# Optimization experiments

Hardware: AMD Instinct MI355X
Metric: run time of the kernel (lower is better)

## Reference

```python
import jax, jax.numpy as jnp
import numpy as np

B, S, D, H = 2, 2048, 768, 12
HD = D // H  # 64
SCALE = jnp.sqrt(jnp.float32(D / H))  # sqrt(head_dim) = 8


def setup_inputs() -> dict:
    key = jax.random.key(0)
    ks = jax.random.split(key, 11)
    s = 1.0 / np.sqrt(D)
    inp = {
        'Q': jax.random.normal(ks[0], (B, S, D), jnp.float32),
        'K': jax.random.normal(ks[1], (B, S, D), jnp.float32),
        'V': jax.random.normal(ks[2], (B, S, D), jnp.float32),
        # True = masked out (causal upper triangle), broadcast over heads
        'mask': jnp.broadcast_to(jnp.triu(jnp.ones((S, S), bool), k=1)[None, None], (B, 1, S, S)),
        'Wq': jax.random.uniform(ks[3], (D, D), jnp.float32, -s, s),
        'bq': jax.random.uniform(ks[4], (D,), jnp.float32, -s, s),
        'Wk': jax.random.uniform(ks[5], (D, D), jnp.float32, -s, s),
        'bk': jax.random.uniform(ks[6], (D,), jnp.float32, -s, s),
        'Wv': jax.random.uniform(ks[7], (D, D), jnp.float32, -s, s),
        'bv': jax.random.uniform(ks[8], (D,), jnp.float32, -s, s),
        'Wo': jax.random.uniform(ks[9], (D, D), jnp.float32, -s, s),
        'bo': jax.random.uniform(ks[10], (D,), jnp.float32, -s, s),
    }
    return inp


def _split_heads(x):  # [B,S,D] -> [B,H,S,HD]
    return x.reshape(B, S, H, HD).transpose(0, 2, 1, 3)


def reference(Q, K, V, mask, Wq, bq, Wk, bk, Wv, bv, Wo, bo):
    q = _split_heads(Q @ Wq.T + bq)
    k = _split_heads(K @ Wk.T + bk)
    v = _split_heads(V @ Wv.T + bv)
    # [B,H,S,S] attention scores
    scores = jnp.einsum('bhqd,bhkd->bhqk', q, k) / SCALE
    scores = jnp.where(mask, jnp.float32(-1e9), scores)
    weights = jax.nn.softmax(scores, axis=-1)
    attn = jnp.einsum('bhqk,bhkd->bhqd', weights, v)
    x = attn.transpose(0, 2, 1, 3).reshape(B, S, D)
    x = x @ Wo.T + bo
    return x, weights
```

## Files before the change

### kernel.cpp

```cpp
#include <hip/hip_runtime.h>

#define S_LEN 2048
#define DMODEL 768
#define NHEAD 12
#define BATCH 2
#define BHEADS (BATCH * NHEAD)
#define MROWS (BATCH * S_LEN)
#define X_ELEMS ((size_t)BATCH * S_LEN * DMODEL)
#define W_ELEMS ((size_t)BATCH * NHEAD * S_LEN * S_LEN)
#define WMAT_ELEMS ((size_t)DMODEL * DMODEL)

typedef __attribute__((ext_vector_type(8))) short bf16x8;
typedef __attribute__((ext_vector_type(4))) float f32x4;

__device__ __forceinline__ unsigned short f2bf(float f) {
    union { float f; unsigned int u; } v; v.f = f;
    unsigned int u = v.u;
    return (unsigned short)((u + 0x7FFFu + ((u >> 16) & 1u)) >> 16);
}

__device__ __forceinline__ bf16x8 pack8(float4 a, float4 b) {
    bf16x8 r;
    r[0] = (short)f2bf(a.x); r[1] = (short)f2bf(a.y);
    r[2] = (short)f2bf(a.z); r[3] = (short)f2bf(a.w);
    r[4] = (short)f2bf(b.x); r[5] = (short)f2bf(b.y);
    r[6] = (short)f2bf(b.z); r[7] = (short)f2bf(b.w);
    return r;
}

struct ConvArgs {
    const float* src[7];
    unsigned short* dst[7];
    int n[7];
};

__global__ __launch_bounds__(256) void convert_kernel(ConvArgs a) {
    int t = blockIdx.y;
    int idx = (blockIdx.x * 256 + threadIdx.x) * 8;
    if (idx >= a.n[t]) return;
    const float4* s = (const float4*)(a.src[t] + idx);
    float4 lo = s[0], hi = s[1];
    *(bf16x8*)(a.dst[t] + idx) = pack8(lo, hi);
}

__global__ __launch_bounds__(64) void proj_kernel(
    const unsigned short* __restrict__ A, const unsigned short* __restrict__ W,
    const float* __restrict__ bias, unsigned short* __restrict__ out,
    int mode, float oscale)
{
    int l = threadIdx.x;
    int bm = blockIdx.x & 127;
    int bn = blockIdx.x >> 7;
    int m0 = bm * 32, n0 = bn * 32;
    int lr = l & 15, ks = l >> 4, g = l >> 4;
    const unsigned short* ap = A + (size_t)(m0 + lr) * DMODEL + ks * 8;
    const unsigned short* bp = W + (size_t)(n0 + lr) * DMODEL + ks * 8;
    f32x4 acc00 = {0,0,0,0}, acc01 = {0,0,0,0}, acc10 = {0,0,0,0}, acc11 = {0,0,0,0};
    for (int k0 = 0; k0 < DMODEL; k0 += 32) {
        bf16x8 a0 = *(const bf16x8*)(ap + k0);
        bf16x8 a1 = *(const bf16x8*)(ap + 16 * DMODEL + k0);
        bf16x8 b0 = *(const bf16x8*)(bp + k0);
        bf16x8 b1 = *(const bf16x8*)(bp + 16 * DMODEL + k0);
        acc00 = __builtin_amdgcn_mfma_f32_16x16x32_bf16(a0, b0, acc00, 0, 0, 0);
        acc01 = __builtin_amdgcn_mfma_f32_16x16x32_bf16(a0, b1, acc01, 0, 0, 0);
        acc10 = __builtin_amdgcn_mfma_f32_16x16x32_bf16(a1, b0, acc10, 0, 0, 0);
        acc11 = __builtin_amdgcn_mfma_f32_16x16x32_bf16(a1, b1, acc11, 0, 0, 0);
    }
    f32x4 accs[2][2] = {{acc00, acc01}, {acc10, acc11}};
#pragma unroll
    for (int mi = 0; mi < 2; ++mi) {
#pragma unroll
        for (int ni = 0; ni < 2; ++ni) {
            int ng = n0 + ni * 16 + lr;
            int h = ng >> 6, d = ng & 63;
            float bv = bias[ng];
#pragma unroll
            for (int i = 0; i < 4; ++i) {
                int mg = m0 + mi * 16 + g * 4 + i;
                int b = mg >> 11, s = mg & 2047;
                float val = (accs[mi][ni][i] + bv) * oscale;
                size_t idx;
                if (mode == 0) idx = ((size_t)(b * NHEAD + h) * S_LEN + s) * 64 + d;
                else           idx = ((size_t)(b * NHEAD + h) * 64 + d) * S_LEN + s;
                out[idx] = f2bf(val);
            }
        }
    }
}

__global__ __launch_bounds__(256) void zero_upper_kernel(float* __restrict__ wts) {
    int qblk = blockIdx.x >> 5, tcol = blockIdx.x & 31;
    if (tcol <= qblk) return;
    int bh = blockIdx.y;
    int tid = threadIdx.x;
    float4 z = {0.f, 0.f, 0.f, 0.f};
    float* base = wts + ((size_t)bh * S_LEN + qblk * 64) * S_LEN + tcol * 64;
#pragma unroll
    for (int it = 0; it < 4; ++it) {
        int r = it * 16 + (tid >> 4);
        *(float4*)&base[(size_t)r * S_LEN + (tid & 15) * 4] = z;
    }
}

__global__ __launch_bounds__(256) void attn_fused_kernel(
    const unsigned short* __restrict__ qbuf, const unsigned short* __restrict__ kbuf,
    const unsigned short* __restrict__ vTbuf, float* __restrict__ wts,
    unsigned short* __restrict__ abuf)
{
    __shared__ unsigned short kt[64 * 72];
    __shared__ unsigned short vt[64 * 72];
    __shared__ unsigned short pt[4 * 16 * 72];
    int tid = threadIdx.x;
    int wid = tid >> 6, l = tid & 63;
    int qblk = blockIdx.x;
    int bh = blockIdx.y;
    int qr0 = qblk * 64 + wid * 16;
    int lr = l & 15, ks = l >> 4, g = l >> 4;

    const unsigned short* qp = qbuf + ((size_t)bh * S_LEN + qr0 + lr) * 64 + ks * 8;
    bf16x8 qf0 = *(const bf16x8*)qp;
    bf16x8 qf1 = *(const bf16x8*)(qp + 32);

    const unsigned short* ksrc = kbuf + (size_t)bh * S_LEN * 64;
    const unsigned short* vsrc = vTbuf + (size_t)bh * 64 * S_LEN;

    auto stageK = [&](int t) {
#pragma unroll
        for (int it = 0; it < 2; ++it) {
            int idx = it * 256 + tid;
            int row = idx >> 3, grp = idx & 7;
            *(bf16x8*)&kt[row * 72 + grp * 8] =
                *(const bf16x8*)&ksrc[(size_t)(t * 64 + row) * 64 + grp * 8];
        }
    };
    auto stageV = [&](int t) {
#pragma unroll
        for (int it = 0; it < 2; ++it) {
            int idx = it * 256 + tid;
            int row = idx >> 3, grp = idx & 7;
            *(bf16x8*)&vt[row * 72 + grp * 8] =
                *(const bf16x8*)&vsrc[(size_t)row * S_LEN + t * 64 + grp * 8];
        }
    };

    float m[4] = {-1e30f, -1e30f, -1e30f, -1e30f};
    float lsum[4] = {0.f, 0.f, 0.f, 0.f};

    for (int t = 0; t < qblk; ++t) {
        __syncthreads(); stageK(t); __syncthreads();
#pragma unroll
        for (int c = 0; c < 4; ++c) {
            const unsigned short* kp = &kt[(c * 16 + lr) * 72 + ks * 8];
            bf16x8 kf0 = *(const bf16x8*)kp;
            bf16x8 kf1 = *(const bf16x8*)(kp + 32);
            f32x4 acc = {0.f, 0.f, 0.f, 0.f};
            acc = __builtin_amdgcn_mfma_f32_16x16x32_bf16(qf0, kf0, acc, 0, 0, 0);
            acc = __builtin_amdgcn_mfma_f32_16x16x32_bf16(qf1, kf1, acc, 0, 0, 0);
#pragma unroll
            for (int i = 0; i < 4; ++i) m[i] = fmaxf(m[i], acc[i]);
        }
    }
    {
        __syncthreads(); stageK(qblk); __syncthreads();
#pragma unroll
        for (int c = 0; c < 4; ++c) {
            const unsigned short* kp = &kt[(c * 16 + lr) * 72 + ks * 8];
            bf16x8 kf0 = *(const bf16x8*)kp;
            bf16x8 kf1 = *(const bf16x8*)(kp + 32);
            f32x4 acc = {0.f, 0.f, 0.f, 0.f};
            acc = __builtin_amdgcn_mfma_f32_16x16x32_bf16(qf0, kf0, acc, 0, 0, 0);
            acc = __builtin_amdgcn_mfma_f32_16x16x32_bf16(qf1, kf1, acc, 0, 0, 0);
            int kcol = qblk * 64 + c * 16 + lr;
#pragma unroll
            for (int i = 0; i < 4; ++i)
                if (kcol <= qr0 + g * 4 + i) m[i] = fmaxf(m[i], acc[i]);
        }
    }
#pragma unroll
    for (int i = 0; i < 4; ++i) {
        m[i] = fmaxf(m[i], __shfl_xor(m[i], 1));
        m[i] = fmaxf(m[i], __shfl_xor(m[i], 2));
        m[i] = fmaxf(m[i], __shfl_xor(m[i], 4));
        m[i] = fmaxf(m[i], __shfl_xor(m[i], 8));
    }

    for (int t = 0; t < qblk; ++t) {
        __syncthreads(); stageK(t); __syncthreads();
#pragma unroll
        for (int c = 0; c < 4; ++c) {
            const unsigned short* kp = &kt[(c * 16 + lr) * 72 + ks * 8];
            bf16x8 kf0 = *(const bf16x8*)kp;
            bf16x8 kf1 = *(const bf16x8*)(kp + 32);
            f32x4 acc = {0.f, 0.f, 0.f, 0.f};
            acc = __builtin_amdgcn_mfma_f32_16x16x32_bf16(qf0, kf0, acc, 0, 0, 0);
            acc = __builtin_amdgcn_mfma_f32_16x16x32_bf16(qf1, kf1, acc, 0, 0, 0);
#pragma unroll
            for (int i = 0; i < 4; ++i) lsum[i] += __expf(acc[i] - m[i]);
        }
    }
    {
        __syncthreads(); stageK(qblk); __syncthreads();
#pragma unroll
        for (int c = 0; c < 4; ++c) {
            const unsigned short* kp = &kt[(c * 16 + lr) * 72 + ks * 8];
            bf16x8 kf0 = *(const bf16x8*)kp;
            bf16x8 kf1 = *(const bf16x8*)(kp + 32);
            f32x4 acc = {0.f, 0.f, 0.f, 0.f};
            acc = __builtin_amdgcn_mfma_f32_16x16x32_bf16(qf0, kf0, acc, 0, 0, 0);
            acc = __builtin_amdgcn_mfma_f32_16x16x32_bf16(qf1, kf1, acc, 0, 0, 0);
            int kcol = qblk * 64 + c * 16 + lr;
#pragma unroll
            for (int i = 0; i < 4; ++i)
                if (kcol <= qr0 + g * 4 + i) lsum[i] += __expf(acc[i] - m[i]);
        }
    }
#pragma unroll
    for (int i = 0; i < 4; ++i) {
        lsum[i] += __shfl_xor(lsum[i], 1);
        lsum[i] += __shfl_xor(lsum[i], 2);
        lsum[i] += __shfl_xor(lsum[i], 4);
        lsum[i] += __shfl_xor(lsum[i], 8);
    }
    float invl[4];
#pragma unroll
    for (int i = 0; i < 4; ++i) invl[i] = 1.0f / lsum[i];

    f32x4 oacc[4] = {{0,0,0,0},{0,0,0,0},{0,0,0,0},{0,0,0,0}};
    unsigned short* ptw = &pt[wid * 16 * 72];
    for (int t = 0; t <= qblk; ++t) {
        __syncthreads(); stageK(t); stageV(t); __syncthreads();
        bool dg = (t == qblk);
#pragma unroll
        for (int c = 0; c < 4; ++c) {
            const unsigned short* kp = &kt[(c * 16 + lr) * 72 + ks * 8];
            bf16x8 kf0 = *(const bf16x8*)kp;
            bf16x8 kf1 = *(const bf16x8*)(kp + 32);
            f32x4 acc = {0.f, 0.f, 0.f, 0.f};
            acc = __builtin_amdgcn_mfma_f32_16x16x32_bf16(qf0, kf0, acc, 0, 0, 0);
            acc = __builtin_amdgcn_mfma_f32_16x16x32_bf16(qf1, kf1, acc, 0, 0, 0);
            int kcol = t * 64 + c * 16 + lr;
#pragma unroll
            for (int i = 0; i < 4; ++i) {
                int qrow = qr0 + g * 4 + i;
                float w = (!dg || kcol <= qrow) ? __expf(acc[i] - m[i]) * invl[i] : 0.f;
                wts[((size_t)bh * S_LEN + qrow) * S_LEN + kcol] = w;
                ptw[(g * 4 + i) * 72 + c * 16 + lr] = f2bf(w);
            }
        }
        bf16x8 pa0 = *(bf16x8*)&ptw[lr * 72 + ks * 8];
        bf16x8 pa1 = *(bf16x8*)&ptw[lr * 72 + 32 + ks * 8];
#pragma unroll
        for (int dt = 0; dt < 4; ++dt) {
            bf16x8 vb0 = *(bf16x8*)&vt[(dt * 16 + lr) * 72 + ks * 8];
            bf16x8 vb1 = *(bf16x8*)&vt[(dt * 16 + lr) * 72 + 32 + ks * 8];
            oacc[dt] = __builtin_amdgcn_mfma_f32_16x16x32_bf16(pa0, vb0, oacc[dt], 0, 0, 0);
            oacc[dt] = __builtin_amdgcn_mfma_f32_16x16x32_bf16(pa1, vb1, oacc[dt], 0, 0, 0);
        }
    }
    int b = bh / NHEAD, h = bh % NHEAD;
#pragma unroll
    for (int dt = 0; dt < 4; ++dt) {
#pragma unroll
        for (int i = 0; i < 4; ++i) {
            int s = qr0 + g * 4 + i;
            abuf[(((size_t)b * S_LEN + s) * NHEAD + h) * 64 + dt * 16 + lr] = f2bf(oacc[dt][i]);
        }
    }
}

__global__ __launch_bounds__(64) void out_proj_kernel(
    const unsigned short* __restrict__ A, const unsigned short* __restrict__ W,
    const float* __restrict__ bias, float* __restrict__ out)
{
    int l = threadIdx.x;
    int bm = blockIdx.x & 127, bn = blockIdx.x >> 7;
    int m0 = bm * 32, n0 = bn * 32;
    int lr = l & 15, ks = l >> 4, g = l >> 4;
    const unsigned short* ap = A + (size_t)(m0 + lr) * DMODEL + ks * 8;
    const unsigned short* bp = W + (size_t)(n0 + lr) * DMODEL + ks * 8;
    f32x4 acc00 = {0,0,0,0}, acc01 = {0,0,0,0}, acc10 = {0,0,0,0}, acc11 = {0,0,0,0};
    for (int k0 = 0; k0 < DMODEL; k0 += 32) {
        bf16x8 a0 = *(const bf16x8*)(ap + k0);
        bf16x8 a1 = *(const bf16x8*)(ap + 16 * DMODEL + k0);
        bf16x8 b0 = *(const bf16x8*)(bp + k0);
        bf16x8 b1 = *(const bf16x8*)(bp + 16 * DMODEL + k0);
        acc00 = __builtin_amdgcn_mfma_f32_16x16x32_bf16(a0, b0, acc00, 0, 0, 0);
        acc01 = __builtin_amdgcn_mfma_f32_16x16x32_bf16(a0, b1, acc01, 0, 0, 0);
        acc10 = __builtin_amdgcn_mfma_f32_16x16x32_bf16(a1, b0, acc10, 0, 0, 0);
        acc11 = __builtin_amdgcn_mfma_f32_16x16x32_bf16(a1, b1, acc11, 0, 0, 0);
    }
    f32x4 accs[2][2] = {{acc00, acc01}, {acc10, acc11}};
#pragma unroll
    for (int mi = 0; mi < 2; ++mi) {
#pragma unroll
        for (int ni = 0; ni < 2; ++ni) {
            int ng = n0 + ni * 16 + lr;
            float bv = bias[ng];
#pragma unroll
            for (int i = 0; i < 4; ++i) {
                int mg = m0 + mi * 16 + g * 4 + i;
                out[(size_t)mg * DMODEL + ng] = accs[mi][ni][i] + bv;
            }
        }
    }
}

extern "C" void kernel_launch(void* const* d_in, const int* in_sizes, int n_in,
                              void* d_out, int out_size, void* d_ws, size_t ws_size,
                              hipStream_t stream) {
    const float* Q  = (const float*)d_in[0];
    const float* K  = (const float*)d_in[1];
    const float* V  = (const float*)d_in[2];
    const float* Wq = (const float*)d_in[4];
    const float* bq = (const float*)d_in[5];
    const float* Wk = (const float*)d_in[6];
    const float* bk = (const float*)d_in[7];
    const float* Wv = (const float*)d_in[8];
    const float* bv = (const float*)d_in[9];
    const float* Wo = (const float*)d_in[10];
    const float* bo = (const float*)d_in[11];

    float* xout = (float*)d_out;
    float* wts  = xout + X_ELEMS;

    unsigned short* p = (unsigned short*)d_ws;
    unsigned short* Qb   = p; p += X_ELEMS;
    unsigned short* Kb   = p; p += X_ELEMS;
    unsigned short* Vb   = p; p += X_ELEMS;
    unsigned short* Wqb  = p; p += WMAT_ELEMS;
    unsigned short* Wkb  = p; p += WMAT_ELEMS;
    unsigned short* Wvb  = p; p += WMAT_ELEMS;
    unsigned short* Wob  = p; p += WMAT_ELEMS;
    unsigned short* qbuf = p; p += X_ELEMS;
    unsigned short* kbuf = p; p += X_ELEMS;
    unsigned short* vT   = p; p += X_ELEMS;
    unsigned short* abuf = p; p += X_ELEMS;

    ConvArgs ca;
    ca.src[0] = Q;  ca.dst[0] = Qb;  ca.n[0] = (int)X_ELEMS;
    ca.src[1] = K;  ca.dst[1] = Kb;  ca.n[1] = (int)X_ELEMS;
    ca.src[2] = V;  ca.dst[2] = Vb;  ca.n[2] = (int)X_ELEMS;
    ca.src[3] = Wq; ca.dst[3] = Wqb; ca.n[3] = (int)WMAT_ELEMS;
    ca.src[4] = Wk; ca.dst[4] = Wkb; ca.n[4] = (int)WMAT_ELEMS;
    ca.src[5] = Wv; ca.dst[5] = Wvb; ca.n[5] = (int)WMAT_ELEMS;
    ca.src[6] = Wo; ca.dst[6] = Wob; ca.n[6] = (int)WMAT_ELEMS;
    convert_kernel<<<dim3(1536, 7), 256, 0, stream>>>(ca);

    const int PROJ_GRID = 128 * 24;
    proj_kernel<<<PROJ_GRID, 64, 0, stream>>>(Qb, Wqb, bq, qbuf, 0, 0.125f);
    proj_kernel<<<PROJ_GRID, 64, 0, stream>>>(Kb, Wkb, bk, kbuf, 0, 1.0f);
    proj_kernel<<<PROJ_GRID, 64, 0, stream>>>(Vb, Wvb, bv, vT,   1, 1.0f);

    zero_upper_kernel<<<dim3(32 * 32, 24), 256, 0, stream>>>(wts);

    attn_fused_kernel<<<dim3(32, 24), 256, 0, stream>>>(qbuf, kbuf, vT, wts, abuf);

    out_proj_kernel<<<PROJ_GRID, 64, 0, stream>>>(abuf, Wob, bo, xout);
}
```

Baseline: 725.6 us.

## Tile projection GEMMs in LDS and use online-softmax attention with 128-row query blocks

Replaces the per-wave 32x32 projection kernels with a 256-thread 128x128 LDS-tiled GEMM that prefetches the next K slice into registers, and uses the same kernel for the output projection. The attention kernel changes from three passes (max, sum, output) to two by computing max and sum together online. Each block now handles 128 query rows with 32 rows per wave, and block order is reversed so the longest causal blocks launch first. The aims are better operand reuse, fewer K reloads and recomputed QK products, and less load imbalance. The cost is fewer blocks (192 GEMM blocks and 384 attention blocks), which risks low occupancy and idle compute units.

Result: faster. 672.3 us (-7.3%).

```diff
diff --git a/kernel.cpp b/kernel.cpp
--- a/kernel.cpp
+++ b/kernel.cpp
@@ -4,8 +4,6 @@
 #define DMODEL 768
 #define NHEAD 12
 #define BATCH 2
-#define BHEADS (BATCH * NHEAD)
-#define MROWS (BATCH * S_LEN)
 #define X_ELEMS ((size_t)BATCH * S_LEN * DMODEL)
 #define W_ELEMS ((size_t)BATCH * NHEAD * S_LEN * S_LEN)
 #define WMAT_ELEMS ((size_t)DMODEL * DMODEL)
@@ -28,6 +26,19 @@
     return r;
 }
 
+__device__ __forceinline__ float rmax16(float v) {
+    v = fmaxf(v, __shfl_xor(v, 1));
+    v = fmaxf(v, __shfl_xor(v, 2));
+    v = fmaxf(v, __shfl_xor(v, 4));
+    v = fmaxf(v, __shfl_xor(v, 8));
+    return v;
+}
+__device__ __forceinline__ float rsum16(float v) {
+    v += __shfl_xor(v, 1); v += __shfl_xor(v, 2);
+    v += __shfl_xor(v, 4); v += __shfl_xor(v, 8);
+    return v;
+}
+
 struct ConvArgs {
     const float* src[7];
     unsigned short* dst[7];
@@ -43,49 +54,81 @@
     *(bf16x8*)(a.dst[t] + idx) = pack8(lo, hi);
 }
 
-__global__ __launch_bounds__(64) void proj_kernel(
-    const unsigned short* __restrict__ A, const unsigned short* __restrict__ W,
-    const float* __restrict__ bias, unsigned short* __restrict__ out,
-    int mode, float oscale)
+__global__ __launch_bounds__(256) void gemm_kernel(
+    const unsigned short* __restrict__ A, const unsigned short* __restrict__ Bw,
+    const float* __restrict__ bias, unsigned short* __restrict__ outb,
+    float* __restrict__ outf, int mode, float oscale)
 {
-    int l = threadIdx.x;
-    int bm = blockIdx.x & 127;
-    int bn = blockIdx.x >> 7;
-    int m0 = bm * 32, n0 = bn * 32;
+    __shared__ unsigned short As[128 * 40];
+    __shared__ unsigned short Bs[128 * 40];
+    int tid = threadIdx.x;
+    int bm = blockIdx.x & 31, bn = blockIdx.x >> 5;
+    int m0 = bm * 128, n0 = bn * 128;
+    int wid = tid >> 6, l = tid & 63;
+    int wr = wid >> 1, wc = wid & 1;
     int lr = l & 15, ks = l >> 4, g = l >> 4;
-    const unsigned short* ap = A + (size_t)(m0 + lr) * DMODEL + ks * 8;
-    const unsigned short* bp = W + (size_t)(n0 + lr) * DMODEL + ks * 8;
-    f32x4 acc00 = {0,0,0,0}, acc01 = {0,0,0,0}, acc10 = {0,0,0,0}, acc11 = {0,0,0,0};
-    for (int k0 = 0; k0 < DMODEL; k0 += 32) {
-        bf16x8 a0 = *(const bf16x8*)(ap + k0);
-        bf16x8 a1 = *(const bf16x8*)(ap + 16 * DMODEL + k0);
-        bf16x8 b0 = *(const bf16x8*)(bp + k0);
-        bf16x8 b1 = *(const bf16x8*)(bp + 16 * DMODEL + k0);
-        acc00 = __builtin_amdgcn_mfma_f32_16x16x32_bf16(a0, b0, acc00, 0, 0, 0);
-        acc01 = __builtin_amdgcn_mfma_f32_16x16x32_bf16(a0, b1, acc01, 0, 0, 0);
-        acc10 = __builtin_amdgcn_mfma_f32_16x16x32_bf16(a1, b0, acc10, 0, 0, 0);
-        acc11 = __builtin_amdgcn_mfma_f32_16x16x32_bf16(a1, b1, acc11, 0, 0, 0);
-    }
-    f32x4 accs[2][2] = {{acc00, acc01}, {acc10, acc11}};
-#pragma unroll
-    for (int mi = 0; mi < 2; ++mi) {
-#pragma unroll
-        for (int ni = 0; ni < 2; ++ni) {
-            int ng = n0 + ni * 16 + lr;
-            int h = ng >> 6, d = ng & 63;
-            float bv = bias[ng];
+
+    int srow = tid >> 1, scg = (tid & 1) * 16;
+    const unsigned short* aptr = A + (size_t)(m0 + srow) * DMODEL + scg;
+    const unsigned short* bptr = Bw + (size_t)(n0 + srow) * DMODEL + scg;
+    unsigned short* adst = &As[srow * 40 + scg];
+    unsigned short* bdst = &Bs[srow * 40 + scg];
+
+    bf16x8 ar0 = *(const bf16x8*)aptr, ar1 = *(const bf16x8*)(aptr + 8);
+    bf16x8 br0 = *(const bf16x8*)bptr, br1 = *(const bf16x8*)(bptr + 8);
+
+    f32x4 acc[4][4];
+#pragma unroll
+    for (int mi = 0; mi < 4; ++mi)
+#pragma unroll
+        for (int ni = 0; ni < 4; ++ni) acc[mi][ni] = (f32x4){0.f, 0.f, 0.f, 0.f};
+
+    for (int kk = 0; kk < 24; ++kk) {
+        __syncthreads();
+        *(bf16x8*)adst = ar0; *(bf16x8*)(adst + 8) = ar1;
+        *(bf16x8*)bdst = br0; *(bf16x8*)(bdst + 8) = br1;
+        __syncthreads();
+        if (kk < 23) {
+            int k0 = (kk + 1) * 32;
+            ar0 = *(const bf16x8*)(aptr + k0); ar1 = *(const bf16x8*)(aptr + k0 + 8);
+            br0 = *(const bf16x8*)(bptr + k0); br1 = *(const bf16x8*)(bptr + k0 + 8);
+        }
+        bf16x8 af[4], bf_[4];
+#pragma unroll
+        for (int mi = 0; mi < 4; ++mi)
+            af[mi] = *(const bf16x8*)&As[(wr * 64 + mi * 16 + lr) * 40 + ks * 8];
+#pragma unroll
+        for (int ni = 0; ni < 4; ++ni)
+            bf_[ni] = *(const bf16x8*)&Bs[(wc * 64 + ni * 16 + lr) * 40 + ks * 8];
+#pragma unroll
+        for (int mi = 0; mi < 4; ++mi)
+#pragma unroll
+            for (int ni = 0; ni < 4; ++ni)
+                acc[mi][ni] = __builtin_amdgcn_mfma_f32_16x16x32_bf16(af[mi], bf_[ni], acc[mi][ni], 0, 0, 0);
+    }
+
+#pragma unroll
+    for (int mi = 0; mi < 4; ++mi)
+#pragma unroll
+        for (int ni = 0; ni < 4; ++ni) {
+            int ngl = n0 + wc * 64 + ni * 16 + lr;
+            float bv = bias[ngl];
+            int h = ngl >> 6, d = ngl & 63;
 #pragma unroll
             for (int i = 0; i < 4; ++i) {
-                int mg = m0 + mi * 16 + g * 4 + i;
-                int b = mg >> 11, s = mg & 2047;
-                float val = (accs[mi][ni][i] + bv) * oscale;
-                size_t idx;
-                if (mode == 0) idx = ((size_t)(b * NHEAD + h) * S_LEN + s) * 64 + d;
-                else           idx = ((size_t)(b * NHEAD + h) * 64 + d) * S_LEN + s;
-                out[idx] = f2bf(val);
-            }
-        }
-    }
+                int mg = m0 + wr * 64 + mi * 16 + g * 4 + i;
+                float val = (acc[mi][ni][i] + bv) * oscale;
+                if (mode == 0) {
+                    int b = mg >> 11, s = mg & 2047;
+                    outb[((size_t)(b * NHEAD + h) * S_LEN + s) * 64 + d] = f2bf(val);
+                } else if (mode == 1) {
+                    int b = mg >> 11, s = mg & 2047;
+                    outb[((size_t)(b * NHEAD + h) * 64 + d) * S_LEN + s] = f2bf(val);
+                } else {
+                    outf[(size_t)mg * DMODEL + ngl] = val;
+                }
+            }
+        }
 }
 
 __global__ __launch_bounds__(256) void zero_upper_kernel(float* __restrict__ wts) {
@@ -109,200 +152,193 @@
 {
     __shared__ unsigned short kt[64 * 72];
     __shared__ unsigned short vt[64 * 72];
-    __shared__ unsigned short pt[4 * 16 * 72];
+    __shared__ unsigned short pt[128 * 72];
     int tid = threadIdx.x;
     int wid = tid >> 6, l = tid & 63;
-    int qblk = blockIdx.x;
+    int qblk = 15 - blockIdx.x;
     int bh = blockIdx.y;
-    int qr0 = qblk * 64 + wid * 16;
+    int qb0 = qblk * 128;
+    int qr0 = qb0 + wid * 32;
     int lr = l & 15, ks = l >> 4, g = l >> 4;
-
-    const unsigned short* qp = qbuf + ((size_t)bh * S_LEN + qr0 + lr) * 64 + ks * 8;
-    bf16x8 qf0 = *(const bf16x8*)qp;
-    bf16x8 qf1 = *(const bf16x8*)(qp + 32);
+    int nt = 2 * qblk + 2;
+    int tmaxw = (qr0 + 31) >> 6;
 
     const unsigned short* ksrc = kbuf + (size_t)bh * S_LEN * 64;
     const unsigned short* vsrc = vTbuf + (size_t)bh * 64 * S_LEN;
 
-    auto stageK = [&](int t) {
-#pragma unroll
-        for (int it = 0; it < 2; ++it) {
-            int idx = it * 256 + tid;
-            int row = idx >> 3, grp = idx & 7;
-            *(bf16x8*)&kt[row * 72 + grp * 8] =
-                *(const bf16x8*)&ksrc[(size_t)(t * 64 + row) * 64 + grp * 8];
-        }
-    };
-    auto stageV = [&](int t) {
-#pragma unroll
-        for (int it = 0; it < 2; ++it) {
-            int idx = it * 256 + tid;
-            int row = idx >> 3, grp = idx & 7;
-            *(bf16x8*)&vt[row * 72 + grp * 8] =
-                *(const bf16x8*)&vsrc[(size_t)row * S_LEN + t * 64 + grp * 8];
-        }
-    };
-
-    float m[4] = {-1e30f, -1e30f, -1e30f, -1e30f};
-    float lsum[4] = {0.f, 0.f, 0.f, 0.f};
-
-    for (int t = 0; t < qblk; ++t) {
-        __syncthreads(); stageK(t); __syncthreads();
+    bf16x8 qf[2][2];
+#pragma unroll
+    for (int mi = 0; mi < 2; ++mi) {
+        const unsigned short* qp = qbuf + ((size_t)bh * S_LEN + qr0 + mi * 16 + lr) * 64 + ks * 8;
+        qf[mi][0] = *(const bf16x8*)qp;
+        qf[mi][1] = *(const bf16x8*)(qp + 32);
+    }
+
+    int srow = tid >> 2, sgrp = (tid & 3) * 16;
+    const unsigned short* kstage = ksrc + (size_t)srow * 64 + sgrp;
+    const unsigned short* vstage = vsrc + (size_t)srow * S_LEN + sgrp;
+    unsigned short* kdst = &kt[srow * 72 + sgrp];
+    unsigned short* vdst = &vt[srow * 72 + sgrp];
+    unsigned short* ptw = &pt[(wid * 32) * 72];
+
+    float m[2][4], lsum[2][4];
+#pragma unroll
+    for (int mi = 0; mi < 2; ++mi)
+#pragma unroll
+        for (int i = 0; i < 4; ++i) { m[mi][i] = -1e30f; lsum[mi][i] = 0.f; }
+
+    bf16x8 kr0 = *(const bf16x8*)kstage;
+    bf16x8 kr1 = *(const bf16x8*)(kstage + 8);
+    for (int t = 0; t < nt; ++t) {
+        __syncthreads();
+        *(bf16x8*)kdst = kr0; *(bf16x8*)(kdst + 8) = kr1;
+        __syncthreads();
+        if (t + 1 < nt) {
+            kr0 = *(const bf16x8*)(kstage + (size_t)(t + 1) * 4096);
+            kr1 = *(const bf16x8*)(kstage + (size_t)(t + 1) * 4096 + 8);
+        }
+        if (t > tmaxw) continue;
+        f32x4 accs[2][4];
 #pragma unroll
         for (int c = 0; c < 4; ++c) {
-            const unsigned short* kp = &kt[(c * 16 + lr) * 72 + ks * 8];
-            bf16x8 kf0 = *(const bf16x8*)kp;
-            bf16x8 kf1 = *(const bf16x8*)(kp + 32);
-            f32x4 acc = {0.f, 0.f, 0.f, 0.f};
-            acc = __builtin_amdgcn_mfma_f32_16x16x32_bf16(qf0, kf0, acc, 0, 0, 0);
-            acc = __builtin_amdgcn_mfma_f32_16x16x32_bf16(qf1, kf1, acc, 0, 0, 0);
-#pragma unroll
-            for (int i = 0; i < 4; ++i) m[i] = fmaxf(m[i], acc[i]);
-        }
-    }
-    {
-        __syncthreads(); stageK(qblk); __syncthreads();
+            bf16x8 kf0 = *(const bf16x8*)&kt[(c * 16 + lr) * 72 + ks * 8];
+            bf16x8 kf1 = *(const bf16x8*)&kt[(c * 16 + lr) * 72 + 32 + ks * 8];
+#pragma unroll
+            for (int mi = 0; mi < 2; ++mi) {
+                f32x4 a = {0.f, 0.f, 0.f, 0.f};
+                a = __builtin_amdgcn_mfma_f32_16x16x32_bf16(qf[mi][0], kf0, a, 0, 0, 0);
+                a = __builtin_amdgcn_mfma_f32_16x16x32_bf16(qf[mi][1], kf1, a, 0, 0, 0);
+                accs[mi][c] = a;
+            }
+        }
+        if (t == tmaxw) {
+#pragma unroll
+            for (int c = 0; c < 4; ++c) {
+                int kcol = t * 64 + c * 16 + lr;
+#pragma unroll
+                for (int mi = 0; mi < 2; ++mi)
+#pragma unroll
+                    for (int i = 0; i < 4; ++i)
+                        if (kcol > qr0 + mi * 16 + g * 4 + i) accs[mi][c][i] = -1e30f;
+            }
+        }
+#pragma unroll
+        for (int mi = 0; mi < 2; ++mi)
+#pragma unroll
+            for (int i = 0; i < 4; ++i) {
+                float a0 = accs[mi][0][i], a1 = accs[mi][1][i];
+                float a2 = accs[mi][2][i], a3 = accs[mi][3][i];
+                float tm = fmaxf(fmaxf(a0, a1), fmaxf(a2, a3));
+                float mn = fmaxf(m[mi][i], tm);
+                float ls = lsum[mi][i] * __expf(m[mi][i] - mn);
+                float p0 = __expf(a0 - mn); if (a0 < -5e29f) p0 = 0.f;
+                float p1 = __expf(a1 - mn); if (a1 < -5e29f) p1 = 0.f;
+                float p2 = __expf(a2 - mn); if (a2 < -5e29f) p2 = 0.f;
+                float p3 = __expf(a3 - mn); if (a3 < -5e29f) p3 = 0.f;
+                lsum[mi][i] = ls + (p0 + p1) + (p2 + p3);
+                m[mi][i] = mn;
+            }
+    }
+
+    float invl[2][4];
+#pragma unroll
+    for (int mi = 0; mi < 2; ++mi)
+#pragma unroll
+        for (int i = 0; i < 4; ++i) {
+            float mf = rmax16(m[mi][i]);
+            float ls = lsum[mi][i] * __expf(m[mi][i] - mf);
+            ls = rsum16(ls);
+            invl[mi][i] = 1.0f / ls;
+            m[mi][i] = mf;
+        }
+
+    f32x4 oacc[2][4];
+#pragma unroll
+    for (int mi = 0; mi < 2; ++mi)
+#pragma unroll
+        for (int dt = 0; dt < 4; ++dt) oacc[mi][dt] = (f32x4){0.f, 0.f, 0.f, 0.f};
+
+    kr0 = *(const bf16x8*)kstage;
+    kr1 = *(const bf16x8*)(kstage + 8);
+    bf16x8 vr0 = *(const bf16x8*)vstage;
+    bf16x8 vr1 = *(const bf16x8*)(vstage + 8);
+    for (int t = 0; t < nt; ++t) {
+        __syncthreads();
+        *(bf16x8*)kdst = kr0; *(bf16x8*)(kdst + 8) = kr1;
+        *(bf16x8*)vdst = vr0; *(bf16x8*)(vdst + 8) = vr1;
+        __syncthreads();
+        if (t + 1 < nt) {
+            kr0 = *(const bf16x8*)(kstage + (size_t)(t + 1) * 4096);
+            kr1 = *(const bf16x8*)(kstage + (size_t)(t + 1) * 4096 + 8);
+            vr0 = *(const bf16x8*)(vstage + (t + 1) * 64);
+            vr1 = *(const bf16x8*)(vstage + (t + 1) * 64 + 8);
+        }
+        if (t > tmaxw) continue;
+        f32x4 accs[2][4];
 #pragma unroll
         for (int c = 0; c < 4; ++c) {
-            const unsigned short* kp = &kt[(c * 16 + lr) * 72 + ks * 8];
-            bf16x8 kf0 = *(const bf16x8*)kp;
-            bf16x8 kf1 = *(const bf16x8*)(kp + 32);
-            f32x4 acc = {0.f, 0.f, 0.f, 0.f};
-            acc = __builtin_amdgcn_mfma_f32_16x16x32_bf16(qf0, kf0, acc, 0, 0, 0);
-            acc = __builtin_amdgcn_mfma_f32_16x16x32_bf16(qf1, kf1, acc, 0, 0, 0);
-            int kcol = qblk * 64 + c * 16 + lr;
-#pragma unroll
-            for (int i = 0; i < 4; ++i)
-                if (kcol <= qr0 + g * 4 + i) m[i] = fmaxf(m[i], acc[i]);
-        }
-    }
-#pragma unroll
-    for (int i = 0; i < 4; ++i) {
-        m[i] = fmaxf(m[i], __shfl_xor(m[i], 1));
-        m[i] = fmaxf(m[i], __shfl_xor(m[i], 2));
-        m[i] = fmaxf(m[i], __shfl_xor(m[i], 4));
-        m[i] = fmaxf(m[i], __shfl_xor(m[i], 8));
-    }
-
-    for (int t = 0; t < qblk; ++t) {
-        __syncthreads(); stageK(t); __syncthreads();
+            bf16x8 kf0 = *(const bf16x8*)&kt[(c * 16 + lr) * 72 + ks * 8];
+            bf16x8 kf1 = *(const bf16x8*)&kt[(c * 16 + lr) * 72 + 32 + ks * 8];
+#pragma unroll
+            for (int mi = 0; mi < 2; ++mi) {
+                f32x4 a = {0.f, 0.f, 0.f, 0.f};
+                a = __builtin_amdgcn_mfma_f32_16x16x32_bf16(qf[mi][0], kf0, a, 0, 0, 0);
+                a = __builtin_amdgcn_mfma_f32_16x16x32_bf16(qf[mi][1], kf1, a, 0, 0, 0);
+                accs[mi][c] = a;
+            }
+        }
+        if (t == tmaxw) {
+#pragma unroll
+            for (int c = 0; c < 4; ++c) {
+                int kcol = t * 64 + c * 16 + lr;
+#pragma unroll
+                for (int mi = 0; mi < 2; ++mi)
+#pragma unroll
+                    for (int i = 0; i < 4; ++i)
+                        if (kcol > qr0 + mi * 16 + g * 4 + i) accs[mi][c][i] = -1e30f;
+            }
+        }
 #pragma unroll
         for (int c = 0; c < 4; ++c) {
-            const unsigned short* kp = &kt[(c * 16 + lr) * 72 + ks * 8];
-            bf16x8 kf0 = *(const bf16x8*)kp;
-            bf16x8 kf1 = *(const bf16x8*)(kp + 32);
-            f32x4 acc = {0.f, 0.f, 0.f, 0.f};
-            acc = __builtin_amdgcn_mfma_f32_16x16x32_bf16(qf0, kf0, acc, 0, 0, 0);
-            acc = __builtin_amdgcn_mfma_f32_16x16x32_bf16(qf1, kf1, acc, 0, 0, 0);
-#pragma unroll
-            for (int i = 0; i < 4; ++i) lsum[i] += __expf(acc[i] - m[i]);
-        }
-    }
-    {
-        __syncthreads(); stageK(qblk); __syncthreads();
-#pragma unroll
-        for (int c = 0; c < 4; ++c) {
-            const unsigned short* kp = &kt[(c * 16 + lr) * 72 + ks * 8];
-            bf16x8 kf0 = *(const bf16x8*)kp;
-            bf16x8 kf1 = *(const bf16x8*)(kp + 32);
-            f32x4 acc = {0.f, 0.f, 0.f, 0.f};
-            acc = __builtin_amdgcn_mfma_f32_16x16x32_bf16(qf0, kf0, acc, 0, 0, 0);
-            acc = __builtin_amdgcn_mfma_f32_16x16x32_bf16(qf1, kf1, acc, 0, 0, 0);
-            int kcol = qblk * 64 + c * 16 + lr;
-#pragma unroll
-            for (int i = 0; i < 4; ++i)
-                if (kcol <= qr0 + g * 4 + i) lsum[i] += __expf(acc[i] - m[i]);
-        }
-    }
-#pragma unroll
-    for (int i = 0; i < 4; ++i) {
-        lsum[i] += __shfl_xor(lsum[i], 1);
-        lsum[i] += __shfl_xor(lsum[i], 2);
-        lsum[i] += __shfl_xor(lsum[i], 4);
-        lsum[i] += __shfl_xor(lsum[i], 8);
-    }
-    float invl[4];
-#pragma unroll
-    for (int i = 0; i < 4; ++i) invl[i] = 1.0f / lsum[i];
-
-    f32x4 oacc[4] = {{0,0,0,0},{0,0,0,0},{0,0,0,0},{0,0,0,0}};
-    unsigned short* ptw = &pt[wid * 16 * 72];
-    for (int t = 0; t <= qblk; ++t) {
-        __syncthreads(); stageK(t); stageV(t); __syncthreads();
-        bool dg = (t == qblk);
-#pragma unroll
-        for (int c = 0; c < 4; ++c) {
-            const unsigned short* kp = &kt[(c * 16 + lr) * 72 + ks * 8];
-            bf16x8 kf0 = *(const bf16x8*)kp;
-            bf16x8 kf1 = *(const bf16x8*)(kp + 32);
-            f32x4 acc = {0.f, 0.f, 0.f, 0.f};
-            acc = __builtin_amdgcn_mfma_f32_16x16x32_bf16(qf0, kf0, acc, 0, 0, 0);
-            acc = __builtin_amdgcn_mfma_f32_16x16x32_bf16(qf1, kf1, acc, 0, 0, 0);
             int kcol = t * 64 + c * 16 + lr;
 #pragma unroll
+            for (int mi = 0; mi < 2; ++mi)
+#pragma unroll
+                for (int i = 0; i < 4; ++i) {
+                    int qrow = qr0 + mi * 16 + g * 4 + i;
+                    float w = __expf(accs[mi][c][i] - m[mi][i]) * invl[mi][i];
+                    wts[((size_t)bh * S_LEN + qrow) * S_LEN + kcol] = w;
+                    ptw[(mi * 16 + g * 4 + i) * 72 + c * 16 + lr] = f2bf(w);
+                }
+        }
+        bf16x8 pa[2][2];
+#pragma unroll
+        for (int mi = 0; mi < 2; ++mi) {
+            pa[mi][0] = *(const bf16x8*)&ptw[(mi * 16 + lr) * 72 + ks * 8];
+            pa[mi][1] = *(const bf16x8*)&ptw[(mi * 16 + lr) * 72 + 32 + ks * 8];
+        }
+#pragma unroll
+        for (int dt = 0; dt < 4; ++dt) {
+            bf16x8 vb0 = *(const bf16x8*)&vt[(dt * 16 + lr) * 72 + ks * 8];
+            bf16x8 vb1 = *(const bf16x8*)&vt[(dt * 16 + lr) * 72 + 32 + ks * 8];
+#pragma unroll
+            for (int mi = 0; mi < 2; ++mi) {
+                oacc[mi][dt] = __builtin_amdgcn_mfma_f32_16x16x32_bf16(pa[mi][0], vb0, oacc[mi][dt], 0, 0, 0);
+                oacc[mi][dt] = __builtin_amdgcn_mfma_f32_16x16x32_bf16(pa[mi][1], vb1, oacc[mi][dt], 0, 0, 0);
+            }
+        }
+    }
+
+    int b = bh / NHEAD, h = bh % NHEAD;
+#pragma unroll
+    for (int mi = 0; mi < 2; ++mi)
+#pragma unroll
+        for (int dt = 0; dt < 4; ++dt)
+#pragma unroll
             for (int i = 0; i < 4; ++i) {
-                int qrow = qr0 + g * 4 + i;
-                float w = (!dg || kcol <= qrow) ? __expf(acc[i] - m[i]) * invl[i] : 0.f;
-                wts[((size_t)bh * S_LEN + qrow) * S_LEN + kcol] = w;
-                ptw[(g * 4 + i) * 72 + c * 16 + lr] = f2bf(w);
-            }
-        }
-        bf16x8 pa0 = *(bf16x8*)&ptw[lr * 72 + ks * 8];
-        bf16x8 pa1 = *(bf16x8*)&ptw[lr * 72 + 32 + ks * 8];
-#pragma unroll
-        for (int dt = 0; dt < 4; ++dt) {
-            bf16x8 vb0 = *(bf16x8*)&vt[(dt * 16 + lr) * 72 + ks * 8];
-            bf16x8 vb1 = *(bf16x8*)&vt[(dt * 16 + lr) * 72 + 32 + ks * 8];
-            oacc[dt] = __builtin_amdgcn_mfma_f32_16x16x32_bf16(pa0, vb0, oacc[dt], 0, 0, 0);
-            oacc[dt] = __builtin_amdgcn_mfma_f32_16x16x32_bf16(pa1, vb1, oacc[dt], 0, 0, 0);
-        }
-    }
-    int b = bh / NHEAD, h = bh % NHEAD;
-#pragma unroll
-    for (int dt = 0; dt < 4; ++dt) {
-#pragma unroll
-        for (int i = 0; i < 4; ++i) {
-            int s = qr0 + g * 4 + i;
-            abuf[(((size_t)b * S_LEN + s) * NHEAD + h) * 64 + dt * 16 + lr] = f2bf(oacc[dt][i]);
-        }
-    }
-}
-
-__global__ __launch_bounds__(64) void out_proj_kernel(
-    const unsigned short* __restrict__ A, const unsigned short* __restrict__ W,
-    const float* __restrict__ bias, float* __restrict__ out)
-{
-    int l = threadIdx.x;
-    int bm = blockIdx.x & 127, bn = blockIdx.x >> 7;
-    int m0 = bm * 32, n0 = bn * 32;
-    int lr = l & 15, ks = l >> 4, g = l >> 4;
-    const unsigned short* ap = A + (size_t)(m0 + lr) * DMODEL + ks * 8;
-    const unsigned short* bp = W + (size_t)(n0 + lr) * DMODEL + ks * 8;
-    f32x4 acc00 = {0,0,0,0}, acc01 = {0,0,0,0}, acc10 = {0,0,0,0}, acc11 = {0,0,0,0};
-    for (int k0 = 0; k0 < DMODEL; k0 += 32) {
-        bf16x8 a0 = *(const bf16x8*)(ap + k0);
-        bf16x8 a1 = *(const bf16x8*)(ap + 16 * DMODEL + k0);
-        bf16x8 b0 = *(const bf16x8*)(bp + k0);
-        bf16x8 b1 = *(const bf16x8*)(bp + 16 * DMODEL + k0);
-        acc00 = __builtin_amdgcn_mfma_f32_16x16x32_bf16(a0, b0, acc00, 0, 0, 0);
-        acc01 = __builtin_amdgcn_mfma_f32_16x16x32_bf16(a0, b1, acc01, 0, 0, 0);
-        acc10 = __builtin_amdgcn_mfma_f32_16x16x32_bf16(a1, b0, acc10, 0, 0, 0);
-        acc11 = __builtin_amdgcn_mfma_f32_16x16x32_bf16(a1, b1, acc11, 0, 0, 0);
-    }
-    f32x4 accs[2][2] = {{acc00, acc01}, {acc10, acc11}};
-#pragma unroll
-    for (int mi = 0; mi < 2; ++mi) {
-#pragma unroll
-        for (int ni = 0; ni < 2; ++ni) {
-            int ng = n0 + ni * 16 + lr;
-            float bv = bias[ng];
-#pragma unroll
-            for (int i = 0; i < 4; ++i) {
-                int mg = m0 + mi * 16 + g * 4 + i;
-                out[(size_t)mg * DMODEL + ng] = accs[mi][ni][i] + bv;
-            }
-        }
-    }
+                int s = qr0 + mi * 16 + g * 4 + i;
+                abuf[(((size_t)b * S_LEN + s) * NHEAD + h) * 64 + dt * 16 + lr] = f2bf(oacc[mi][dt][i]);
+            }
 }
 
 extern "C" void kernel_launch(void* const* d_in, const int* in_sizes, int n_in,
@@ -346,14 +382,14 @@
     ca.src[6] = Wo; ca.dst[6] = Wob; ca.n[6] = (int)WMAT_ELEMS;
     convert_kernel<<<dim3(1536, 7), 256, 0, stream>>>(ca);
 
-    const int PROJ_GRID = 128 * 24;
-    proj_kernel<<<PROJ_GRID, 64, 0, stream>>>(Qb, Wqb, bq, qbuf, 0, 0.125f);
-    proj_kernel<<<PROJ_GRID, 64, 0, stream>>>(Kb, Wkb, bk, kbuf, 0, 1.0f);
-    proj_kernel<<<PROJ_GRID, 64, 0, stream>>>(Vb, Wvb, bv, vT,   1, 1.0f);
+    const int GEMM_GRID = 32 * 6;
+    gemm_kernel<<<GEMM_GRID, 256, 0, stream>>>(Qb, Wqb, bq, qbuf, nullptr, 0, 0.125f);
+    gemm_kernel<<<GEMM_GRID, 256, 0, stream>>>(Kb, Wkb, bk, kbuf, nullptr, 0, 1.0f);
+    gemm_kernel<<<GEMM_GRID, 256, 0, stream>>>(Vb, Wvb, bv, vT,   nullptr, 1, 1.0f);
 
     zero_upper_kernel<<<dim3(32 * 32, 24), 256, 0, stream>>>(wts);
 
-    attn_fused_kernel<<<dim3(32, 24), 256, 0, stream>>>(qbuf, kbuf, vT, wts, abuf);
-
-    out_proj_kernel<<<PROJ_GRID, 64, 0, stream>>>(abuf, Wob, bo, xout);
-}
+    attn_fused_kernel<<<dim3(16, 24), 256, 0, stream>>>(qbuf, kbuf, vT, wts, abuf);
+
+    gemm_kernel<<<GEMM_GRID, 256, 0, stream>>>(abuf, Wob, bo, nullptr, xout, 2, 1.0f);
+}
```
